# Kernel tuning notes

Measured on AMD Instinct MI355X. Metric: run time of the kernel, lower is better.

The kernel has to match this reference:

```python
import jax, jax.numpy as jnp
import numpy as np

WS = 7       # window size per spatial dim
SHIFT = 3    # cyclic shift = WS // 2
HEADS = 6


def _rel_pos_index():
    # [N, N] index into the (2*WS-1)^3 relative-position-bias table
    c = np.stack(np.meshgrid(np.arange(WS), np.arange(WS), np.arange(WS), indexing='ij')).reshape(3, -1)
    rel = (c[:, :, None] - c[:, None, :]).transpose(1, 2, 0) + (WS - 1)
    rel[:, :, 0] *= (2 * WS - 1) ** 2
    rel[:, :, 1] *= (2 * WS - 1)
    return rel.sum(-1)


def _attn_mask(D, H, W):
    # shifted-window attention mask: [nW, N, N] with 0 / -100
    img = np.zeros((D, H, W))
    sl = (slice(0, -WS), slice(-WS, -SHIFT), slice(-SHIFT, None))
    cnt = 0
    for d in sl:
        for h in sl:
            for w in sl:
                img[d, h, w] = cnt
                cnt += 1
    m = img.reshape(D // WS, WS, H // WS, WS, W // WS, WS).transpose(0, 2, 4, 1, 3, 5).reshape(-1, WS ** 3)
    return np.where(m[:, None, :] != m[:, :, None], -100.0, 0.0).astype(np.float32)


def _ln(x, g, b):
    mu = x.mean(-1, keepdims=True)
    var = ((x - mu) ** 2).mean(-1, keepdims=True)
    return (x - mu) * jax.lax.rsqrt(var + 1e-5) * g + b


def _win_part(x):
    B, D, H, W, C = x.shape
    x = x.reshape(B, D // WS, WS, H // WS, WS, W // WS, WS, C)
    return x.transpose(0, 1, 3, 5, 2, 4, 6, 7).reshape(B, -1, WS ** 3, C)


def _win_rev(xw, D, H, W):
    B, _, _, C = xw.shape
    x = xw.reshape(B, D // WS, H // WS, W // WS, WS, WS, WS, C)
    return x.transpose(0, 1, 4, 2, 5, 3, 6, 7).reshape(B, D, H, W, C)


def setup_inputs() -> dict:
    key = jax.random.key(0)
    ks = jax.random.split(key, 8)
    C, dff, Nh = 192, 768, HEADS
    s = 0.02
    return {
        'x': jax.random.normal(ks[0], (2, 28, 28, 28, C), jnp.float32),
        'ln1_g': jnp.ones((C,), jnp.float32),
        'ln1_b': jnp.zeros((C,), jnp.float32),
        'qkv_w': jax.random.normal(ks[1], (3 * C, C), jnp.float32) * s,
        'qkv_b': jnp.zeros((3 * C,), jnp.float32),
        'rpb': jax.random.normal(ks[2], ((2 * WS - 1) ** 3, Nh), jnp.float32) * s,
        'proj_w': jax.random.normal(ks[3], (C, C), jnp.float32) * s,
        'proj_b': jnp.zeros((C,), jnp.float32),
        'ln2_g': jnp.ones((C,), jnp.float32),
        'ln2_b': jnp.zeros((C,), jnp.float32),
        'fc1_w': jax.random.normal(ks[4], (dff, C), jnp.float32) * s,
        'fc1_b': jnp.zeros((dff,), jnp.float32),
        'fc2_w': jax.random.normal(ks[5], (C, dff), jnp.float32) * s,
        'fc2_b': jnp.zeros((C,), jnp.float32),
    }


def reference(x, ln1_g, ln1_b, qkv_w, qkv_b, rpb, proj_w, proj_b, ln2_g, ln2_b, fc1_w, fc1_b, fc2_w, fc2_b):
    B, D, H, W, C = x.shape
    hd = C // HEADS
    N = WS ** 3
    idx = jnp.asarray(_rel_pos_index())          # [N, N] int
    mask = jnp.asarray(_attn_mask(D, H, W))      # [nW, N, N]

    shortcut = x
    h = _ln(x, ln1_g, ln1_b)
    h = jnp.roll(h, (-SHIFT, -SHIFT, -SHIFT), axis=(1, 2, 3))
    xw = _win_part(h)                            # [B, nW, N, C]
    nW = xw.shape[1]

    qkv = xw @ qkv_w.T + qkv_b                   # [B, nW, N, 3C]
    qkv = qkv.reshape(B, nW, N, 3, HEADS, hd).transpose(3, 0, 1, 4, 2, 5)  # [3,B,nW,h,N,hd]
    q, k, v = qkv[0], qkv[1], qkv[2]

    scale = hd ** -0.5
    attn = jnp.einsum('bwhnd,bwhmd->bwhnm', q * scale, k)  # [B,nW,h,N,N]
    bias = rpb[idx].transpose(2, 0, 1)           # [h, N, N]
    attn = attn + bias + mask[None, :, None]
    attn = jax.nn.softmax(attn, axis=-1)

    o = jnp.einsum('bwhnm,bwhmd->bwhnd', attn, v)
    o = o.transpose(0, 1, 3, 2, 4).reshape(B, nW, N, C)
    o = o @ proj_w.T + proj_b
    o = _win_rev(o, D, H, W)
    o = jnp.roll(o, (SHIFT, SHIFT, SHIFT), axis=(1, 2, 3))

    x = shortcut + o
    h2 = _ln(x, ln2_g, ln2_b)
    h2 = jax.nn.gelu(h2 @ fc1_w.T + fc1_b, approximate=False)
    return x + (h2 @ fc2_w.T + fc2_b)
```

## Files before the change

kernel.cpp:

```cpp
#include <hip/hip_runtime.h>
#include <hip/hip_bf16.h>
#include <math.h>

typedef __hip_bfloat16 bf16;
typedef unsigned short u16;
typedef __attribute__((ext_vector_type(8))) short bf16x8;
typedef __attribute__((ext_vector_type(4))) float f32x4;
typedef __attribute__((ext_vector_type(16))) float f32x16;
typedef __attribute__((ext_vector_type(4))) unsigned u32x4;

__device__ __forceinline__ float us2f(u16 u) { return __uint_as_float(((unsigned)u) << 16); }
__device__ __forceinline__ u16 f2us(float f) { bf16 h = __float2bfloat16(f); return *(u16*)&h; }

__device__ __forceinline__ float wave_bcast_sum(float v) {
#pragma unroll
    for (int off = 32; off > 0; off >>= 1) v += __shfl_down(v, off);
    return __shfl(v, 0);
}

__device__ __forceinline__ void glds16(const u16* g, u16* l) {
    __builtin_amdgcn_global_load_lds((const __attribute__((address_space(1))) void*)g,
                                     (__attribute__((address_space(3))) void*)l, 16, 0, 0);
}

__global__ __launch_bounds__(256) void k_prep(
    const float* __restrict__ qkv_w, const float* __restrict__ proj_w,
    const float* __restrict__ rpb,
    u16* __restrict__ qkv_wb, u16* __restrict__ proj_wb, float* __restrict__ biasF)
{
    int idx = blockIdx.x * 256 + threadIdx.x;
    if (idx < 110592) { qkv_wb[idx] = f2us(qkv_w[idx]); return; }
    idx -= 110592;
    if (idx < 36864) { proj_wb[idx] = f2us(proj_w[idx]); return; }
    idx -= 36864;
    if (idx >= 6 * 11 * 11 * 1024) return;
    int r16 = idx & 15;
    int lane = (idx >> 4) & 63;
    int cell = idx >> 10;
    int chunk = cell % 11;
    int t2 = cell / 11;
    int tile = t2 % 11;
    int h = t2 / 11;
    int g = r16 >> 2, q = r16 & 3;
    int hi = lane >> 5, l31 = lane & 31;
    int n = tile * 32 + l31;
    int m = chunk * 32 + 4 * hi + 8 * g + q;
    float v = 0.0f;
    if (m < 343 && n < 343) {
        int ni = n / 49, nr = n - ni * 49, nj = nr / 7, nk = nr - nj * 7;
        int mi = m / 49, mr = m - mi * 49, mj = mr / 7, mk = mr - mj * 7;
        int d = (ni - mi) * 169 + (nj - mj) * 13 + (nk - mk) + 1098;
        v = rpb[d * 6 + h] * 5.656854249492381f;
    }
    biasF[idx] = v;
}

__global__ __launch_bounds__(256) void k_f2b2(
    const float* __restrict__ fc1_w, const float* __restrict__ fc2_w,
    u16* __restrict__ fc1_wb, u16* __restrict__ fc2_wb)
{
    int idx = blockIdx.x * 256 + threadIdx.x;
    if (idx < 147456) fc1_wb[idx] = f2us(fc1_w[idx]);
    else fc2_wb[idx - 147456] = f2us(fc2_w[idx - 147456]);
}

__global__ __launch_bounds__(256) void k_ln1_winpart(
    const float* __restrict__ x, const float* __restrict__ g, const float* __restrict__ b,
    u16* __restrict__ out)
{
    int lane = threadIdx.x & 63;
    int t = blockIdx.x * 4 + (threadIdx.x >> 6);
    int bidx = t / (64 * 343);
    int r = t - bidx * (64 * 343);
    int w = r / 343;
    int n = r - w * 343;
    int wd = w >> 4, wh = (w >> 2) & 3, ww = w & 3;
    int i = n / 49, rem = n - i * 49;
    int j = rem / 7, k = rem - j * 7;
    int sd = wd * 7 + i + 3; if (sd >= 28) sd -= 28;
    int sh = wh * 7 + j + 3; if (sh >= 28) sh -= 28;
    int sw = ww * 7 + k + 3; if (sw >= 28) sw -= 28;
    size_t src = ((((size_t)bidx * 28 + sd) * 28 + sh) * 28 + sw) * 192;
    float v0 = x[src + lane], v1 = x[src + lane + 64], v2 = x[src + lane + 128];
    float s  = wave_bcast_sum(v0 + v1 + v2);
    float mu = s * (1.0f / 192.0f);
    float s2 = wave_bcast_sum(v0 * v0 + v1 * v1 + v2 * v2);
    float rs = rsqrtf(s2 * (1.0f / 192.0f) - mu * mu + 1e-5f);
    u16* op = out + (size_t)t * 192;
    op[lane]       = f2us((v0 - mu) * rs * g[lane]       + b[lane]);
    op[lane + 64]  = f2us((v1 - mu) * rs * g[lane + 64]  + b[lane + 64]);
    op[lane + 128] = f2us((v2 - mu) * rs * g[lane + 128] + b[lane + 128]);
}

__global__ __launch_bounds__(256) void k_add_winrev_ln2(
    const float* __restrict__ x, const u16* __restrict__ projw,
    const float* __restrict__ g, const float* __restrict__ b,
    float* __restrict__ x1, u16* __restrict__ h2)
{
    int lane = threadIdx.x & 63;
    int t = blockIdx.x * 4 + (threadIdx.x >> 6);
    int sw_ = t % 28, t1 = t / 28;
    int sh_ = t1 % 28, t2 = t1 / 28;
    int sd_ = t2 % 28, bidx = t2 / 28;
    int rd = sd_ + 25; if (rd >= 28) rd -= 28;
    int rh = sh_ + 25; if (rh >= 28) rh -= 28;
    int rw = sw_ + 25; if (rw >= 28) rw -= 28;
    int wd = rd / 7, i = rd - wd * 7;
    int wh = rh / 7, j = rh - wh * 7;
    int ww = rw / 7, k = rw - ww * 7;
    int w = (wd << 4) + (wh << 2) + ww;
    int n = (i * 7 + j) * 7 + k;
    size_t src = (((size_t)(bidx * 64 + w)) * 343 + n) * 192;
    const float* xp = x + (size_t)t * 192;
    float v0 = xp[lane]       + us2f(projw[src + lane]);
    float v1 = xp[lane + 64]  + us2f(projw[src + lane + 64]);
    float v2 = xp[lane + 128] + us2f(projw[src + lane + 128]);
    float* op = x1 + (size_t)t * 192;
    op[lane] = v0; op[lane + 64] = v1; op[lane + 128] = v2;
    float s  = wave_bcast_sum(v0 + v1 + v2);
    float mu = s * (1.0f / 192.0f);
    float s2 = wave_bcast_sum(v0 * v0 + v1 * v1 + v2 * v2);
    float rs = rsqrtf(s2 * (1.0f / 192.0f) - mu * mu + 1e-5f);
    u16* hp = h2 + (size_t)t * 192;
    hp[lane]       = f2us((v0 - mu) * rs * g[lane]       + b[lane]);
    hp[lane + 64]  = f2us((v1 - mu) * rs * g[lane + 64]  + b[lane + 64]);
    hp[lane + 128] = f2us((v2 - mu) * rs * g[lane + 128] + b[lane + 128]);
}

template<int ACT, int OUT, int GX>
__global__ __launch_bounds__(256) void k_gemm_fs(
    const u16* __restrict__ A, const u16* __restrict__ W, const float* __restrict__ bias,
    u16* __restrict__ outB, float* __restrict__ outF, const float* __restrict__ resid,
    int M, int Nc)
{
    constexpr int K = 192;
    __shared__ __align__(16) u16 As[3][128 * 64];
    __shared__ __align__(16) u16 Bs[3][64 * 64];
    int tid = threadIdx.x;
    int lane = tid & 63, wv = tid >> 6;
    int quad = lane >> 4, l16 = lane & 15;

    int nwg = gridDim.x, orig = blockIdx.x;
    int q = nwg >> 3, r = nwg & 7;
    int xcd = orig & 7, lin = orig >> 3;
    int L = (xcd < r ? xcd * (q + 1) : r * (q + 1) + (xcd - r) * q) + lin;
    int bx = L % GX, by = L / GX;
    int m0 = by << 7, n0 = bx << 6;

    int srow = wv * 8 + (lane >> 3);
    int swz  = ((lane & 7) << 3) ^ (((lane >> 3) & 7) << 3);
    const u16* gA = A + (size_t)(m0 + srow) * K + swz;
    const u16* gB = W + (size_t)(n0 + srow) * K + swz;
    int rsA = 32 * K;

#pragma unroll
    for (int t = 0; t < 3; ++t) {
#pragma unroll
        for (int i = 0; i < 4; i++)
            glds16(gA + (size_t)i * rsA + t * 64, &As[t][(i * 4 + wv) * 512]);
#pragma unroll
        for (int i = 0; i < 2; i++)
            glds16(gB + (size_t)i * rsA + t * 64, &Bs[t][(i * 4 + wv) * 512]);
    }
    asm volatile("s_waitcnt vmcnt(0)" ::: "memory");
    __builtin_amdgcn_s_barrier();

    f32x4 acc[2][4] = {};
    int rswz = (l16 & 7) << 3;
#pragma unroll
    for (int t = 0; t < 3; ++t) {
#pragma unroll
        for (int kk = 0; kk < 2; kk++) {
            int ko = (kk * 32 + quad * 8) ^ rswz;
            bf16x8 af[2], bfr[4];
#pragma unroll
            for (int mt = 0; mt < 2; mt++)
                af[mt] = *(const bf16x8*)&As[t][(wv * 32 + mt * 16 + l16) * 64 + ko];
#pragma unroll
            for (int nt = 0; nt < 4; nt++)
                bfr[nt] = *(const bf16x8*)&Bs[t][(nt * 16 + l16) * 64 + ko];
#pragma unroll
            for (int mt = 0; mt < 2; mt++)
#pragma unroll
                for (int nt = 0; nt < 4; nt++)
                    acc[mt][nt] = __builtin_amdgcn_mfma_f32_16x16x32_bf16(af[mt], bfr[nt], acc[mt][nt], 0, 0, 0);
        }
    }
#pragma unroll
    for (int mt = 0; mt < 2; mt++) {
#pragma unroll
        for (int nt = 0; nt < 4; nt++) {
#pragma unroll
            for (int r2 = 0; r2 < 4; r2++) {
                int m = m0 + wv * 32 + mt * 16 + quad * 4 + r2;
                int n = n0 + nt * 16 + l16;
                float v = acc[mt][nt][r2] + bias[n];
                if (ACT == 1) v = 0.5f * v * (1.0f + erff(v * 0.70710678118654752f));
                size_t off = (size_t)m * Nc + n;
                if (OUT == 1) outB[off] = f2us(v);
                else outF[off] = resid[off] + v;
            }
        }
    }
}

template<int ACT, int OUT, int GX>
__global__ __launch_bounds__(256) void k_gemm_mfma(
    const u16* __restrict__ A, const u16* __restrict__ W, const float* __restrict__ bias,
    u16* __restrict__ outB, float* __restrict__ outF, const float* __restrict__ resid,
    int M, int Nc, int K)
{
    __shared__ __align__(16) u16 As[2][128 * 64];
    __shared__ __align__(16) u16 Bs[2][64 * 64];
    int tid = threadIdx.x;
    int lane = tid & 63, wv = tid >> 6;
    int quad = lane >> 4, l16 = lane & 15;

    int nwg = gridDim.x, orig = blockIdx.x;
    int q = nwg >> 3, r = nwg & 7;
    int xcd = orig & 7, lin = orig >> 3;
    int L = (xcd < r ? xcd * (q + 1) : r * (q + 1) + (xcd - r) * q) + lin;
    int bx = L % GX, by = L / GX;
    int m0 = by << 7, n0 = bx << 6;

    f32x4 acc[2][4] = {};

    int srow = wv * 8 + (lane >> 3);
    int swz  = ((lane & 7) << 3) ^ (((lane >> 3) & 7) << 3);
    const u16* gA = A + (size_t)(m0 + srow) * K + swz;
    const u16* gB = W + (size_t)(n0 + srow) * K + swz;
    int rsA = 32 * K;

    int nst = K >> 6;
#define STAGE(buf, k0)                                                        \
    {                                                                         \
        _Pragma("unroll")                                                     \
        for (int i = 0; i < 4; i++)                                           \
            glds16(gA + (size_t)i * rsA + (k0), &As[buf][(i * 4 + wv) * 512]); \
        _Pragma("unroll")                                                     \
        for (int i = 0; i < 2; i++)                                           \
            glds16(gB + (size_t)i * rsA + (k0), &Bs[buf][(i * 4 + wv) * 512]); \
    }

    STAGE(0, 0);
    asm volatile("s_waitcnt vmcnt(0)" ::: "memory");
    __builtin_amdgcn_s_barrier();

    int rswz = (l16 & 7) << 3;
    int cur = 0;
    for (int t = 0; t < nst; ++t) {
        if (t + 1 < nst) STAGE(cur ^ 1, (t + 1) << 6);
#pragma unroll
        for (int kk = 0; kk < 2; kk++) {
            int ko = (kk * 32 + quad * 8) ^ rswz;
            bf16x8 af[2], bfr[4];
#pragma unroll
            for (int mt = 0; mt < 2; mt++)
                af[mt] = *(const bf16x8*)&As[cur][(wv * 32 + mt * 16 + l16) * 64 + ko];
#pragma unroll
            for (int nt = 0; nt < 4; nt++)
                bfr[nt] = *(const bf16x8*)&Bs[cur][(nt * 16 + l16) * 64 + ko];
#pragma unroll
            for (int mt = 0; mt < 2; mt++)
#pragma unroll
                for (int nt = 0; nt < 4; nt++)
                    acc[mt][nt] = __builtin_amdgcn_mfma_f32_16x16x32_bf16(af[mt], bfr[nt], acc[mt][nt], 0, 0, 0);
        }
        asm volatile("s_waitcnt vmcnt(0)" ::: "memory");
        __builtin_amdgcn_s_barrier();
        cur ^= 1;
    }
#undef STAGE
#pragma unroll
    for (int mt = 0; mt < 2; mt++) {
#pragma unroll
        for (int nt = 0; nt < 4; nt++) {
#pragma unroll
            for (int r2 = 0; r2 < 4; r2++) {
                int m = m0 + wv * 32 + mt * 16 + quad * 4 + r2;
                int n = n0 + nt * 16 + l16;
                float v = acc[mt][nt][r2] + bias[n];
                if (ACT == 1) v = 0.5f * v * (1.0f + erff(v * 0.70710678118654752f));
                size_t off = (size_t)m * Nc + n;
                if (OUT == 1) outB[off] = f2us(v);
                else outF[off] = resid[off] + v;
            }
        }
    }
}

__global__ __launch_bounds__(704, 6) void k_attn(
    const u16* __restrict__ qkv, const float* __restrict__ biasF, u16* __restrict__ o_win)
{
    int head = blockIdx.x;
    int w = blockIdx.y;
    int bidx = blockIdx.z;
    __shared__ __align__(16) u16 Ks[352 * 40];
    __shared__ __align__(16) u16 Vt[32 * 360];
    __shared__ unsigned char lab[352];
    int tid = threadIdx.x;
    int lane = tid & 63, wv = tid >> 6;
    int hi = lane >> 5, l31 = lane & 31;
    size_t base = ((size_t)(bidx * 64 + w)) * 343;

    for (int i = tid; i < 2816; i += 704) {
        int m = i >> 3;
        int d4 = (i & 7) << 2;
        ushort4 kv = {0, 0, 0, 0}, vv = {0, 0, 0, 0};
        if (m < 343) {
            size_t off = (base + m) * 576 + head * 32 + d4;
            kv = *(const ushort4*)(qkv + off + 192);
            vv = *(const ushort4*)(qkv + off + 384);
        }
        *(ushort4*)&Ks[m * 40 + d4] = kv;
        Vt[(d4 + 0) * 360 + m] = vv.x;
        Vt[(d4 + 1) * 360 + m] = vv.y;
        Vt[(d4 + 2) * 360 + m] = vv.z;
        Vt[(d4 + 3) * 360 + m] = vv.w;
    }
    int wd = w >> 4, wh = (w >> 2) & 3, ww = w & 3;
    bool uni = (wd < 3) && (wh < 3) && (ww < 3);
    for (int n = tid; n < 352; n += 704) {
        unsigned char lv = 255;
        if (n < 343) {
            int i = n / 49, rem = n - i * 49;
            int j = rem / 7, k = rem - j * 7;
            int gd = wd * 7 + i, gh = wh * 7 + j, gw = ww * 7 + k;
            int ld_ = (gd < 21) ? 0 : ((gd < 25) ? 1 : 2);
            int lh_ = (gh < 21) ? 0 : ((gh < 25) ? 1 : 2);
            int lw_ = (gw < 21) ? 0 : ((gw < 25) ? 1 : 2);
            lv = (unsigned char)(ld_ * 9 + lh_ * 3 + lw_);
        }
        lab[n] = lv;
    }
    __syncthreads();

    const float SCALE = 0.17677669529663687f;
    const f32x16 z16 = {0,0,0,0,0,0,0,0,0,0,0,0,0,0,0,0};

    int tile = wv;
    int n0 = tile * 32;
    int nq = n0 + l31; if (nq > 342) nq = 342;
    const u16* qp = qkv + (base + nq) * 576 + head * 32;
    bf16x8 bq0 = *(const bf16x8*)(qp + hi * 8);
    bf16x8 bq1 = *(const bf16x8*)(qp + 16 + hi * 8);
    unsigned lr = lab[n0 + l31];
    const float* bfr = biasF + ((size_t)(head * 11 + tile) * 11) * 1024 + lane * 16;

    f32x16 o = z16;
    float psum = 0.0f;

    auto chunk = [&](int c, int mode) {
        int mb = c * 32;
        const u16* kp = &Ks[(mb + l31) * 40 + hi * 8];
        bf16x8 ka0 = *(const bf16x8*)kp;
        bf16x8 ka1 = *(const bf16x8*)(kp + 16);
        f32x16 s;
        const float* bc = bfr + c * 1024;
#pragma unroll
        for (int g = 0; g < 4; ++g)
            ((float4*)&s)[g] = *(const float4*)(bc + g * 4);
        s = __builtin_amdgcn_mfma_f32_32x32x16_bf16(ka0, bq0, s, 0, 0, 0);
        s = __builtin_amdgcn_mfma_f32_32x32x16_bf16(ka1, bq1, s, 0, 0, 0);
        float p[16];
        if (mode == 0) {
#pragma unroll
            for (int r = 0; r < 16; ++r) p[r] = __expf(s[r] * SCALE);
        } else if (mode == 1) {
#pragma unroll
            for (int r = 0; r < 16; ++r) {
                int m = mb + 4 * hi + 8 * (r >> 2) + (r & 3);
                float e = __expf(s[r] * SCALE);
                p[r] = (m < 343) ? e : 0.0f;
            }
        } else {
            unsigned labw[4];
#pragma unroll
            for (int g = 0; g < 4; ++g)
                labw[g] = *(const unsigned*)&lab[mb + hi * 4 + g * 8];
#pragma unroll
            for (int r = 0; r < 16; ++r) {
                float e = __expf(s[r] * SCALE);
                p[r] = (((labw[r >> 2] >> (8 * (r & 3))) & 255u) == lr) ? e : 0.0f;
            }
        }
#pragma unroll
        for (int r = 0; r < 16; ++r) psum += p[r];
        unsigned pk0, pk1, pk2, pk3, pk4, pk5, pk6, pk7;
        asm("v_cvt_pk_bf16_f32 %0, %1, %2" : "=v"(pk0) : "v"(p[0]),  "v"(p[1]));
        asm("v_cvt_pk_bf16_f32 %0, %1, %2" : "=v"(pk1) : "v"(p[2]),  "v"(p[3]));
        asm("v_cvt_pk_bf16_f32 %0, %1, %2" : "=v"(pk2) : "v"(p[4]),  "v"(p[5]));
        asm("v_cvt_pk_bf16_f32 %0, %1, %2" : "=v"(pk3) : "v"(p[6]),  "v"(p[7]));
        asm("v_cvt_pk_bf16_f32 %0, %1, %2" : "=v"(pk4) : "v"(p[8]),  "v"(p[9]));
        asm("v_cvt_pk_bf16_f32 %0, %1, %2" : "=v"(pk5) : "v"(p[10]), "v"(p[11]));
        asm("v_cvt_pk_bf16_f32 %0, %1, %2" : "=v"(pk6) : "v"(p[12]), "v"(p[13]));
        asm("v_cvt_pk_bf16_f32 %0, %1, %2" : "=v"(pk7) : "v"(p[14]), "v"(p[15]));
        asm volatile("v_permlane32_swap_b32 %0, %1" : "+v"(pk0), "+v"(pk2));
        asm volatile("v_permlane32_swap_b32 %0, %1" : "+v"(pk1), "+v"(pk3));
        asm volatile("v_permlane32_swap_b32 %0, %1" : "+v"(pk4), "+v"(pk6));
        asm volatile("v_permlane32_swap_b32 %0, %1" : "+v"(pk5), "+v"(pk7));
        u32x4 A1 = {pk0, pk1, pk2, pk3};
        u32x4 A2 = {pk4, pk5, pk6, pk7};
        bf16x8 pa0 = __builtin_bit_cast(bf16x8, A1);
        bf16x8 pa1 = __builtin_bit_cast(bf16x8, A2);
        const u16* vp = &Vt[l31 * 360 + mb + hi * 8];
        bf16x8 vb0 = *(const bf16x8*)vp;
        bf16x8 vb1 = *(const bf16x8*)(vp + 16);
        o = __builtin_amdgcn_mfma_f32_32x32x16_bf16(pa0, vb0, o, 0, 0, 0);
        o = __builtin_amdgcn_mfma_f32_32x32x16_bf16(pa1, vb1, o, 0, 0, 0);
    };

    if (uni) {
#pragma unroll 2
        for (int c = 0; c < 10; ++c) chunk(c, 0);
        chunk(10, 1);
    } else {
#pragma unroll 2
        for (int c = 0; c < 11; ++c) chunk(c, 2);
    }

    psum += __shfl_xor(psum, 32);
    float inv = 1.0f / psum;
#pragma unroll
    for (int r = 0; r < 16; ++r) {
        int crow = (r & 3) + 8 * (r >> 2) + 4 * hi;
        int n = n0 + crow;
        float invc = __shfl(inv, crow);
        if (n < 343) {
            u16* op = o_win + (base + n) * 192 + head * 32;
            op[l31] = f2us(o[r] * invc);
        }
    }
}

extern "C" void kernel_launch(void* const* d_in, const int* in_sizes, int n_in,
                              void* d_out, int out_size, void* d_ws, size_t ws_size,
                              hipStream_t stream)
{
    const float* x      = (const float*)d_in[0];
    const float* ln1_g  = (const float*)d_in[1];
    const float* ln1_b  = (const float*)d_in[2];
    const float* qkv_w  = (const float*)d_in[3];
    const float* qkv_b  = (const float*)d_in[4];
    const float* rpb    = (const float*)d_in[5];
    const float* proj_w = (const float*)d_in[6];
    const float* proj_b = (const float*)d_in[7];
    const float* ln2_g  = (const float*)d_in[8];
    const float* ln2_b  = (const float*)d_in[9];
    const float* fc1_w  = (const float*)d_in[10];
    const float* fc1_b  = (const float*)d_in[11];
    const float* fc2_w  = (const float*)d_in[12];
    const float* fc2_b  = (const float*)d_in[13];

    const int M = 43904;
    const size_t MC  = (size_t)M * 192;
    const size_t MC2 = MC * 2;

    char* ws = (char*)d_ws;
    u16* hA     = (u16*)ws;
    u16* qkvb   = (u16*)(ws + MC2);
    u16* projw  = (u16*)(ws + MC2);
    u16* gbuf   = (u16*)(ws + MC2);
    u16* fc1_wb = (u16*)(ws + 51u * 1024 * 1024);
    u16* fc2_wb = (u16*)(ws + 51u * 1024 * 1024 + 294912);
    float* out  = (float*)d_out;
    u16* qkv_wb  = (u16*)d_out;
    u16* proj_wb = (u16*)d_out + 110592;
    float* biasF = (float*)((char*)d_out + 4u * 1024 * 1024);

    k_prep<<<3481, 256, 0, stream>>>(qkv_w, proj_w, rpb, qkv_wb, proj_wb, biasF);
    k_ln1_winpart<<<M / 4, 256, 0, stream>>>(x, ln1_g, ln1_b, hA);
    k_gemm_fs<0, 1, 9><<<3087, 256, 0, stream>>>(hA, qkv_wb, qkv_b, qkvb, nullptr, nullptr, M, 576);
    k_attn<<<dim3(6, 64, 2), 704, 0, stream>>>(qkvb, biasF, hA);
    k_f2b2<<<1152, 256, 0, stream>>>(fc1_w, fc2_w, fc1_wb, fc2_wb);
    k_gemm_fs<0, 1, 3><<<1029, 256, 0, stream>>>(hA, proj_wb, proj_b, projw, nullptr, nullptr, M, 192);
    k_add_winrev_ln2<<<M / 4, 256, 0, stream>>>(x, projw, ln2_g, ln2_b, out, hA);
    const int CH0 = 22016, CH1 = 21888;
    k_gemm_fs<1, 1, 12><<<2064, 256, 0, stream>>>(hA, fc1_wb, fc1_b, gbuf, nullptr, nullptr, CH0, 768);
    k_gemm_mfma<0, 2, 3><<<516, 256, 0, stream>>>(gbuf, fc2_wb, fc2_b, nullptr, out, out, CH0, 192, 768);
    k_gemm_fs<1, 1, 12><<<2052, 256, 0, stream>>>(hA + (size_t)CH0 * 192, fc1_wb, fc1_b, gbuf, nullptr, nullptr, CH1, 768);
    k_gemm_mfma<0, 2, 3><<<513, 256, 0, stream>>>(gbuf, fc2_wb, fc2_b, nullptr, out + (size_t)CH0 * 192, out + (size_t)CH0 * 192, CH1, 192, 768);
}
```

Before: 285.0 us.

## Replace full-K LDS staging GEMM with double-buffered 32-wide K pipeline

The K=192 GEMM used for qkv, proj and fc1 previously loaded the whole 128x192 A tile and 64x192 B tile into LDS in one shot before computing. It now streams K in 32-element slices through two LDS buffers, prefetching the next slice while MFMAs run on the current one. This cuts LDS use per block, which can raise occupancy, and overlaps loads with compute. The cost is a barrier and a full vmcnt wait on every K step, plus six serial stages instead of one bulk load.

Result: no change. 287.4 us (+0.8%).

```diff
diff --git a/kernel.cpp b/kernel.cpp
--- a/kernel.cpp
+++ b/kernel.cpp
@@ -128,14 +128,13 @@
 }
 
 template<int ACT, int OUT, int GX>
-__global__ __launch_bounds__(256) void k_gemm_fs(
+__global__ __launch_bounds__(256) void k_gemm32(
     const u16* __restrict__ A, const u16* __restrict__ W, const float* __restrict__ bias,
     u16* __restrict__ outB, float* __restrict__ outF, const float* __restrict__ resid,
-    int M, int Nc)
-{
-    constexpr int K = 192;
-    __shared__ __align__(16) u16 As[3][128 * 64];
-    __shared__ __align__(16) u16 Bs[3][64 * 64];
+    int M, int Nc, int K)
+{
+    __shared__ __align__(16) u16 As[2][128 * 32];
+    __shared__ __align__(16) u16 Bs[2][64 * 32];
     int tid = threadIdx.x;
     int lane = tid & 63, wv = tid >> 6;
     int quad = lane >> 4, l16 = lane & 15;
@@ -147,45 +146,48 @@
     int bx = L % GX, by = L / GX;
     int m0 = by << 7, n0 = bx << 6;
 
-    int srow = wv * 8 + (lane >> 3);
-    int swz  = ((lane & 7) << 3) ^ (((lane >> 3) & 7) << 3);
+    f32x4 acc[2][4] = {};
+
+    int srow = wv * 16 + (lane >> 2);
+    int swz  = ((lane & 3) << 3) ^ (((lane >> 2) & 3) << 3);
     const u16* gA = A + (size_t)(m0 + srow) * K + swz;
     const u16* gB = W + (size_t)(n0 + srow) * K + swz;
-    int rsA = 32 * K;
-
-#pragma unroll
-    for (int t = 0; t < 3; ++t) {
-#pragma unroll
-        for (int i = 0; i < 4; i++)
-            glds16(gA + (size_t)i * rsA + t * 64, &As[t][(i * 4 + wv) * 512]);
-#pragma unroll
-        for (int i = 0; i < 2; i++)
-            glds16(gB + (size_t)i * rsA + t * 64, &Bs[t][(i * 4 + wv) * 512]);
-    }
+    int rsA = 64 * K;
+
+    int nst = K >> 5;
+#define STAGE32(buf, k0)                                                      \
+    {                                                                         \
+        glds16(gA + (k0),                &As[buf][(wv) * 512]);               \
+        glds16(gA + (size_t)rsA + (k0),  &As[buf][(4 + wv) * 512]);           \
+        glds16(gB + (k0),                &Bs[buf][(wv) * 512]);               \
+    }
+
+    STAGE32(0, 0);
     asm volatile("s_waitcnt vmcnt(0)" ::: "memory");
     __builtin_amdgcn_s_barrier();
 
-    f32x4 acc[2][4] = {};
-    int rswz = (l16 & 7) << 3;
-#pragma unroll
-    for (int t = 0; t < 3; ++t) {
-#pragma unroll
-        for (int kk = 0; kk < 2; kk++) {
-            int ko = (kk * 32 + quad * 8) ^ rswz;
-            bf16x8 af[2], bfr[4];
-#pragma unroll
-            for (int mt = 0; mt < 2; mt++)
-                af[mt] = *(const bf16x8*)&As[t][(wv * 32 + mt * 16 + l16) * 64 + ko];
+    int rswz = (l16 & 3) << 3;
+    int cur = 0;
+    for (int t = 0; t < nst; ++t) {
+        if (t + 1 < nst) STAGE32(cur ^ 1, (t + 1) << 5);
+        int ko = (quad * 8) ^ rswz;
+        bf16x8 af[2], bfr[4];
+#pragma unroll
+        for (int mt = 0; mt < 2; mt++)
+            af[mt] = *(const bf16x8*)&As[cur][(wv * 32 + mt * 16 + l16) * 32 + ko];
+#pragma unroll
+        for (int nt = 0; nt < 4; nt++)
+            bfr[nt] = *(const bf16x8*)&Bs[cur][(nt * 16 + l16) * 32 + ko];
+#pragma unroll
+        for (int mt = 0; mt < 2; mt++)
 #pragma unroll
             for (int nt = 0; nt < 4; nt++)
-                bfr[nt] = *(const bf16x8*)&Bs[t][(nt * 16 + l16) * 64 + ko];
-#pragma unroll
-            for (int mt = 0; mt < 2; mt++)
-#pragma unroll
-                for (int nt = 0; nt < 4; nt++)
-                    acc[mt][nt] = __builtin_amdgcn_mfma_f32_16x16x32_bf16(af[mt], bfr[nt], acc[mt][nt], 0, 0, 0);
-        }
-    }
+                acc[mt][nt] = __builtin_amdgcn_mfma_f32_16x16x32_bf16(af[mt], bfr[nt], acc[mt][nt], 0, 0, 0);
+        asm volatile("s_waitcnt vmcnt(0)" ::: "memory");
+        __builtin_amdgcn_s_barrier();
+        cur ^= 1;
+    }
+#undef STAGE32
 #pragma unroll
     for (int mt = 0; mt < 2; mt++) {
 #pragma unroll
@@ -470,14 +472,14 @@
 
     k_prep<<<3481, 256, 0, stream>>>(qkv_w, proj_w, rpb, qkv_wb, proj_wb, biasF);
     k_ln1_winpart<<<M / 4, 256, 0, stream>>>(x, ln1_g, ln1_b, hA);
-    k_gemm_fs<0, 1, 9><<<3087, 256, 0, stream>>>(hA, qkv_wb, qkv_b, qkvb, nullptr, nullptr, M, 576);
+    k_gemm32<0, 1, 9><<<3087, 256, 0, stream>>>(hA, qkv_wb, qkv_b, qkvb, nullptr, nullptr, M, 576, 192);
     k_attn<<<dim3(6, 64, 2), 704, 0, stream>>>(qkvb, biasF, hA);
     k_f2b2<<<1152, 256, 0, stream>>>(fc1_w, fc2_w, fc1_wb, fc2_wb);
-    k_gemm_fs<0, 1, 3><<<1029, 256, 0, stream>>>(hA, proj_wb, proj_b, projw, nullptr, nullptr, M, 192);
+    k_gemm32<0, 1, 3><<<1029, 256, 0, stream>>>(hA, proj_wb, proj_b, projw, nullptr, nullptr, M, 192, 192);
     k_add_winrev_ln2<<<M / 4, 256, 0, stream>>>(x, projw, ln2_g, ln2_b, out, hA);
     const int CH0 = 22016, CH1 = 21888;
-    k_gemm_fs<1, 1, 12><<<2064, 256, 0, stream>>>(hA, fc1_wb, fc1_b, gbuf, nullptr, nullptr, CH0, 768);
+    k_gemm32<1, 1, 12><<<2064, 256, 0, stream>>>(hA, fc1_wb, fc1_b, gbuf, nullptr, nullptr, CH0, 768, 192);
     k_gemm_mfma<0, 2, 3><<<516, 256, 0, stream>>>(gbuf, fc2_wb, fc2_b, nullptr, out, out, CH0, 192, 768);
-    k_gemm_fs<1, 1, 12><<<2052, 256, 0, stream>>>(hA + (size_t)CH0 * 192, fc1_wb, fc1_b, gbuf, nullptr, nullptr, CH1, 768);
+    k_gemm32<1, 1, 12><<<2052, 256, 0, stream>>>(hA + (size_t)CH0 * 192, fc1_wb, fc1_b, gbuf, nullptr, nullptr, CH1, 768, 192);
     k_gemm_mfma<0, 2, 3><<<513, 256, 0, stream>>>(gbuf, fc2_wb, fc2_b, nullptr, out + (size_t)CH0 * 192, out + (size_t)CH0 * 192, CH1, 192, 768);
 }
```
